# Kernel optimization log

Measured on AMD Instinct MI355X. Metric: run time of the kernel, lower is better.

The kernel has to match this reference:

```python
import jax, jax.numpy as jnp
import numpy as np

B, N, DIN, DOUT, H = 4, 2048, 256, 256, 4
HD = DOUT // H
NEG_SLOPE = 0.2


def setup_inputs() -> dict:
    key = jax.random.key(0)
    k1, k2, k3, k4, k5 = jax.random.split(key, 5)
    x = jax.random.normal(k1, (B, N, DIN), dtype=jnp.float32)
    adj = jax.random.randint(k2, (B, N, N), 0, 2).astype(jnp.float32)
    # ensure self-loops so every softmax row has at least one valid entry
    adj = jnp.maximum(adj, jnp.eye(N, dtype=jnp.float32)[None])
    # xavier-uniform-ish scales
    w_bound = float(np.sqrt(6.0 / (DIN + DOUT)))
    a_bound = float(np.sqrt(6.0 / (1 + HD)))
    W = jax.random.uniform(k3, (DOUT, DIN), jnp.float32, -w_bound, w_bound)
    a_src = jax.random.uniform(k4, (H, HD), jnp.float32, -a_bound, a_bound)
    a_dst = jax.random.uniform(k5, (H, HD), jnp.float32, -a_bound, a_bound)
    return {"x": x, "adj": adj, "W": W, "a_src": a_src, "a_dst": a_dst}


def reference(x, adj, W, a_src, a_dst):
    b, n, _ = x.shape
    h = (x @ W.T).reshape(b, n, H, HD)                      # [B,N,H,HD]
    s_src = jnp.einsum('bnhd,hd->bnh', h, a_src)            # [B,N,H]
    s_dst = jnp.einsum('bnhd,hd->bnh', h, a_dst)            # [B,N,H]
    # e[b,i,j,h] = leaky_relu(s_src[b,i,h] + s_dst[b,j,h])
    e = jax.nn.leaky_relu(s_src[:, :, None, :] + s_dst[:, None, :, :], NEG_SLOPE)
    e = jnp.where(adj[..., None] == 0, -jnp.inf, e)         # [B,N,N,H]
    alpha = jax.nn.softmax(e, axis=2)                       # softmax over j (dropout is identity at eval)
    out = jnp.einsum('bijh,bjhd->bihd', alpha, h)           # weighted aggregate
    return out.reshape(b, n, DOUT)
```

## Files before the change

kernel.cpp:

```cpp
#include <hip/hip_runtime.h>
#include <math.h>

#define Bb   4
#define Nn   2048
#define Dd   256
#define Hh   4
#define HDd  64
#define BN   (Bb * Nn)

typedef float v4f __attribute__((ext_vector_type(4)));
typedef short v8s __attribute__((ext_vector_type(8)));

__device__ __forceinline__ unsigned rne_bf16(float f) {
    unsigned u = __float_as_uint(f);
    u += 0x7fffu + ((u >> 16) & 1u);
    return u >> 16;
}

__global__ __launch_bounds__(256, 2) void k_gemm(const float* __restrict__ x,
                                                 const float* __restrict__ W,
                                                 const float* __restrict__ a_src,
                                                 const float* __restrict__ a_dst,
                                                 const float* __restrict__ adj,
                                                 unsigned short* __restrict__ hbf,
                                                 float* __restrict__ ssrc,
                                                 float* __restrict__ sdst,
                                                 unsigned long long* __restrict__ bitadj) {
    __shared__ __align__(16) unsigned short xs[2][64 * 72];
    __shared__ __align__(16) unsigned short wsm[2][64 * 72];
    __shared__ float asd[128];

    const int bid0 = (int)blockIdx.x;
    if (bid0 & 1) {
        const int gw = (bid0 >> 1) * 4 + ((int)threadIdx.x >> 6);
        const int lane = (int)threadIdx.x & 63;
#pragma unroll 1
        for (int w = gw * 4; w < 262144; w += 2048 * 4) {
            float v0 = adj[(size_t)((w + 0) >> 5) * 2048 + ((w + 0) & 31) * 64 + lane];
            float v1 = adj[(size_t)((w + 1) >> 5) * 2048 + ((w + 1) & 31) * 64 + lane];
            float v2 = adj[(size_t)((w + 2) >> 5) * 2048 + ((w + 2) & 31) * 64 + lane];
            float v3 = adj[(size_t)((w + 3) >> 5) * 2048 + ((w + 3) & 31) * 64 + lane];
            unsigned long long m0 = __ballot(v0 != 0.0f);
            unsigned long long m1 = __ballot(v1 != 0.0f);
            unsigned long long m2 = __ballot(v2 != 0.0f);
            unsigned long long m3 = __ballot(v3 != 0.0f);
            if (lane == 0) {
                bitadj[w + 0] = m0;
                bitadj[w + 1] = m1;
                bitadj[w + 2] = m2;
                bitadj[w + 3] = m3;
            }
        }
        return;
    }

    const int g = bid0 >> 1;
    const int head = (g >> 2) & 3;
    const int mtile = (g & 3) + 4 * (g >> 4);
    const int tid = threadIdx.x;
    const int m0 = mtile * 64;
    const int n0 = head * 64;
    const int b = m0 >> 11;
    const int i0loc = m0 & 2047;

    if (tid < 128) {
        int sel = tid >> 6, d = tid & 63;
        asd[tid] = sel ? a_dst[n0 + d] : a_src[n0 + d];
    }

    const int wv = tid >> 6, ln = tid & 63, l15 = ln & 15, l4 = ln >> 4;
    const int mh = wv >> 1, nh = wv & 1;
    const int srow = tid >> 2, kq = (tid & 3) * 16;

    v4f acc[2][2];
#pragma unroll
    for (int gg = 0; gg < 2; ++gg)
#pragma unroll
        for (int t = 0; t < 2; ++t) acc[gg][t] = (v4f){0.f, 0.f, 0.f, 0.f};

    for (int st = 0; st < 4; ++st) {
        const int k0 = st * 64;
        __syncthreads();
        {
            float xf[16], wf[16];
            const float* xp = x + (size_t)(m0 + srow) * Dd + k0 + kq;
            const float* wp = W + (size_t)(n0 + srow) * Dd + k0 + kq;
#pragma unroll
            for (int q = 0; q < 4; ++q) {
                *(float4*)&xf[q * 4] = *(const float4*)(xp + q * 4);
                *(float4*)&wf[q * 4] = *(const float4*)(wp + q * 4);
            }
            unsigned xh[8], xl[8], wh[8], wl[8];
#pragma unroll
            for (int j = 0; j < 8; ++j) {
                unsigned h0 = rne_bf16(xf[2 * j]), h1 = rne_bf16(xf[2 * j + 1]);
                float l0 = xf[2 * j] - __uint_as_float(h0 << 16);
                float l1 = xf[2 * j + 1] - __uint_as_float(h1 << 16);
                xh[j] = h0 | (h1 << 16);
                xl[j] = rne_bf16(l0) | (rne_bf16(l1) << 16);
                unsigned g0 = rne_bf16(wf[2 * j]), g1 = rne_bf16(wf[2 * j + 1]);
                float m0f = wf[2 * j] - __uint_as_float(g0 << 16);
                float m1f = wf[2 * j + 1] - __uint_as_float(g1 << 16);
                wh[j] = g0 | (g1 << 16);
                wl[j] = rne_bf16(m0f) | (rne_bf16(m1f) << 16);
            }
            *(uint4*)(xs[0] + srow * 72 + kq)     = make_uint4(xh[0], xh[1], xh[2], xh[3]);
            *(uint4*)(xs[0] + srow * 72 + kq + 8) = make_uint4(xh[4], xh[5], xh[6], xh[7]);
            *(uint4*)(xs[1] + srow * 72 + kq)     = make_uint4(xl[0], xl[1], xl[2], xl[3]);
            *(uint4*)(xs[1] + srow * 72 + kq + 8) = make_uint4(xl[4], xl[5], xl[6], xl[7]);
            *(uint4*)(wsm[0] + srow * 72 + kq)     = make_uint4(wh[0], wh[1], wh[2], wh[3]);
            *(uint4*)(wsm[0] + srow * 72 + kq + 8) = make_uint4(wh[4], wh[5], wh[6], wh[7]);
            *(uint4*)(wsm[1] + srow * 72 + kq)     = make_uint4(wl[0], wl[1], wl[2], wl[3]);
            *(uint4*)(wsm[1] + srow * 72 + kq + 8) = make_uint4(wl[4], wl[5], wl[6], wl[7]);
        }
        __syncthreads();
        {
            v8s ah[2][2], al[2][2], bh_[2][2], bl_[2][2];
#pragma unroll
            for (int gg = 0; gg < 2; ++gg)
#pragma unroll
                for (int kh = 0; kh < 2; ++kh) {
                    int ro = (mh * 32 + gg * 16 + l15) * 72 + kh * 32 + l4 * 8;
                    ah[gg][kh] = *(const v8s*)(xs[0] + ro);
                    al[gg][kh] = *(const v8s*)(xs[1] + ro);
                }
#pragma unroll
            for (int t = 0; t < 2; ++t)
#pragma unroll
                for (int kh = 0; kh < 2; ++kh) {
                    int ro = (nh * 32 + t * 16 + l15) * 72 + kh * 32 + l4 * 8;
                    bh_[t][kh] = *(const v8s*)(wsm[0] + ro);
                    bl_[t][kh] = *(const v8s*)(wsm[1] + ro);
                }
#pragma unroll
            for (int gg = 0; gg < 2; ++gg)
#pragma unroll
                for (int t = 0; t < 2; ++t)
#pragma unroll
                    for (int kh = 0; kh < 2; ++kh) {
                        acc[gg][t] = __builtin_amdgcn_mfma_f32_16x16x32_bf16(ah[gg][kh], bh_[t][kh], acc[gg][t], 0, 0, 0);
                        acc[gg][t] = __builtin_amdgcn_mfma_f32_16x16x32_bf16(al[gg][kh], bh_[t][kh], acc[gg][t], 0, 0, 0);
                        acc[gg][t] = __builtin_amdgcn_mfma_f32_16x16x32_bf16(ah[gg][kh], bl_[t][kh], acc[gg][t], 0, 0, 0);
                    }
        }
    }

    __syncthreads();
    float* T = (float*)&xs[0][0];
#pragma unroll
    for (int gg = 0; gg < 2; ++gg)
#pragma unroll
        for (int t = 0; t < 2; ++t)
#pragma unroll
            for (int r = 0; r < 4; ++r) {
                int d = nh * 32 + t * 16 + l15;
                int m = mh * 32 + gg * 16 + l4 * 4 + r;
                T[d * 67 + m] = acc[gg][t][r];
            }
    __syncthreads();
    if (tid < 128) {
        int m = tid & 63, sel = tid >> 6;
        float s = 0.f;
#pragma unroll
        for (int d = 0; d < 64; ++d) s += T[d * 67 + m] * asd[sel * 64 + d];
        (sel ? sdst : ssrc)[(size_t)head * BN + (size_t)b * Nn + i0loc + m] = s;
        int dloc = tid >> 1, jh2 = tid & 1;
        const float* row = T + dloc * 67 + jh2 * 32;
        unsigned pk[16];
#pragma unroll
        for (int jj = 0; jj < 16; ++jj)
            pk[jj] = rne_bf16(row[jj * 2]) | (rne_bf16(row[jj * 2 + 1]) << 16);
        const int jb = (i0loc >> 5) + jh2;
        const int dt = dloc >> 4, fl = dloc & 15;
        unsigned short* rb = hbf +
            ((size_t)((b * 64 + jb) * 4 + head) * 2048 + dt * 512 + fl * 8);
        *(uint4*)(rb + 0 * 128) = make_uint4(pk[0],  pk[1],  pk[2],  pk[3]);
        *(uint4*)(rb + 1 * 128) = make_uint4(pk[4],  pk[5],  pk[6],  pk[7]);
        *(uint4*)(rb + 2 * 128) = make_uint4(pk[8],  pk[9],  pk[10], pk[11]);
        *(uint4*)(rb + 3 * 128) = make_uint4(pk[12], pk[13], pk[14], pk[15]);
    }
}

__global__ __launch_bounds__(512, 4) void k_aggr(const unsigned short* __restrict__ hbf,
                                                 const unsigned long long* __restrict__ bitadj,
                                                 const float* __restrict__ ssrc,
                                                 const float* __restrict__ sdst,
                                                 float* __restrict__ out) {
    __shared__ __align__(16) unsigned short Btile[2][2][2048];
    __shared__ __align__(16) float dtab[2048 * 2];
    __shared__ __align__(16) float red[4][64][20];

    const int tid = threadIdx.x;
    const int bid = (int)blockIdx.x;
    const int xcd  = bid & 7;
    const int h    = xcd >> 1;
    const int bpar = xcd & 1;
    const int q    = bid >> 3;
    const int b    = ((q & 1) << 1) | bpar;
    const int itile = q >> 1;
    const int i0 = itile * 64;

    const int wv   = tid >> 6;
    const int isub = wv >> 1;
    const int jp   = wv & 1;
    const int ln = tid & 63, l15 = ln & 15, l4 = ln >> 4;

    const int spar = tid >> 8;
    const int soff = tid & 255;

    {
        const int j4 = tid * 4;
        float4 sv = *(const float4*)(sdst + (size_t)h * BN + (size_t)b * Nn + j4);
        float4 o0 = make_float4(__expf(sv.x), __expf(0.2f * sv.x),
                                __expf(sv.y), __expf(0.2f * sv.y));
        float4 o1 = make_float4(__expf(sv.z), __expf(0.2f * sv.z),
                                __expf(sv.w), __expf(0.2f * sv.w));
        *(float4*)&dtab[j4 * 2]     = o0;
        *(float4*)&dtab[j4 * 2 + 4] = o1;
    }

    const int irow = i0 + isub * 16 + l15;
    const float ss = ssrc[(size_t)h * BN + (size_t)b * Nn + irow];
    const float c1 = __expf(ss), c2 = __expf(0.2f * ss);
    const unsigned char* ajr = (const unsigned char*)bitadj +
        ((size_t)b * Nn + irow) * 256;
    const unsigned short* sbase = hbf +
        ((size_t)(b * 64 * 4) + h) * 2048 + (size_t)soff * 8;
    const float* dtb = dtab + l4 * 16;

    const v8s ones = {0x3F80, 0x3F80, 0x3F80, 0x3F80, 0x3F80, 0x3F80, 0x3F80, 0x3F80};

    v4f acc0 = (v4f){0.f, 0.f, 0.f, 0.f}, acc1 = acc0, acc2 = acc0, acc3 = acc0, zac = acc0;
    uint4 stg;
    unsigned mA, mB;

#define GENFRAG(dst, M_, dd_) do {                                            \
        const float4 q0_ = *(const float4*)((dd_) + 0);                       \
        const float4 q1_ = *(const float4*)((dd_) + 4);                       \
        const float4 q2_ = *(const float4*)((dd_) + 8);                       \
        const float4 q3_ = *(const float4*)((dd_) + 12);                      \
        float w0_ = ((M_) & 1u)   ? fmaxf(c1 * q0_.x, c2 * q0_.y) : 0.f;      \
        float w1_ = ((M_) & 2u)   ? fmaxf(c1 * q0_.z, c2 * q0_.w) : 0.f;      \
        float w2_ = ((M_) & 4u)   ? fmaxf(c1 * q1_.x, c2 * q1_.y) : 0.f;      \
        float w3_ = ((M_) & 8u)   ? fmaxf(c1 * q1_.z, c2 * q1_.w) : 0.f;      \
        float w4_ = ((M_) & 16u)  ? fmaxf(c1 * q2_.x, c2 * q2_.y) : 0.f;      \
        float w5_ = ((M_) & 32u)  ? fmaxf(c1 * q2_.z, c2 * q2_.w) : 0.f;      \
        float w6_ = ((M_) & 64u)  ? fmaxf(c1 * q3_.x, c2 * q3_.y) : 0.f;      \
        float w7_ = ((M_) & 128u) ? fmaxf(c1 * q3_.z, c2 * q3_.w) : 0.f;      \
        union { v8s v; unsigned u[4]; } P_;                                   \
        asm("v_cvt_pk_bf16_f32 %0, %1, %2" : "=v"(P_.u[0]) : "v"(w0_), "v"(w1_)); \
        asm("v_cvt_pk_bf16_f32 %0, %1, %2" : "=v"(P_.u[1]) : "v"(w2_), "v"(w3_)); \
        asm("v_cvt_pk_bf16_f32 %0, %1, %2" : "=v"(P_.u[2]) : "v"(w4_), "v"(w5_)); \
        asm("v_cvt_pk_bf16_f32 %0, %1, %2" : "=v"(P_.u[3]) : "v"(w6_), "v"(w7_)); \
        dst = P_.v;                                                           \
    } while (0)

#define COMPUTE(JC_, M_, btp) do {                                            \
        const unsigned short* bp_ = (btp);                                    \
        v8s bf0_ = *(const v8s*)(bp_ + 0 * 512 + ln * 8);                     \
        v8s bf1_ = *(const v8s*)(bp_ + 1 * 512 + ln * 8);                     \
        v8s bf2_ = *(const v8s*)(bp_ + 2 * 512 + ln * 8);                     \
        v8s bf3_ = *(const v8s*)(bp_ + 3 * 512 + ln * 8);                     \
        const float* dd_ = dtb + (JC_) * 64;                                  \
        v8s afr_;                                                             \
        GENFRAG(afr_, M_, dd_);                                               \
        acc0 = __builtin_amdgcn_mfma_f32_16x16x32_bf16(afr_, bf0_, acc0, 0, 0, 0); \
        acc1 = __builtin_amdgcn_mfma_f32_16x16x32_bf16(afr_, bf1_, acc1, 0, 0, 0); \
        acc2 = __builtin_amdgcn_mfma_f32_16x16x32_bf16(afr_, bf2_, acc2, 0, 0, 0); \
        acc3 = __builtin_amdgcn_mfma_f32_16x16x32_bf16(afr_, bf3_, acc3, 0, 0, 0); \
        zac  = __builtin_amdgcn_mfma_f32_16x16x32_bf16(afr_, ones, zac,  0, 0, 0); \
    } while (0)

    stg = *(const uint4*)(sbase + (size_t)spar * 8192);
    mA = ajr[jp * 4 + l4];
    *(uint4*)&Btile[0][spar][soff * 8] = stg;
    __syncthreads();

#pragma unroll 1
    for (int rr = 0; rr < 32; rr += 2) {
        {
            const int sjc = (2 * rr + 2 + spar) & 63;
            stg = *(const uint4*)(sbase + (size_t)sjc * 8192);
            mB = ajr[((2 * rr + 2 + jp) & 63) * 4 + l4];
            __builtin_amdgcn_sched_barrier(0);
            COMPUTE(2 * rr + jp, mA, Btile[0][jp]);
            *(uint4*)&Btile[1][spar][soff * 8] = stg;
            __syncthreads();
        }
        {
            const int sjc = (2 * rr + 4 + spar) & 63;
            stg = *(const uint4*)(sbase + (size_t)sjc * 8192);
            mA = ajr[((2 * rr + 4 + jp) & 63) * 4 + l4];
            __builtin_amdgcn_sched_barrier(0);
            COMPUTE(2 * rr + 2 + jp, mB, Btile[1][jp]);
            *(uint4*)&Btile[0][spar][soff * 8] = stg;
            __syncthreads();
        }
    }

#undef GENFRAG
#undef COMPUTE

    if (jp) {
        float* rp = &red[isub][ln][0];
        *(v4f*)(rp + 0)  = acc0;
        *(v4f*)(rp + 4)  = acc1;
        *(v4f*)(rp + 8)  = acc2;
        *(v4f*)(rp + 12) = acc3;
        *(v4f*)(rp + 16) = zac;
    }
    __syncthreads();
    if (!jp) {
        const float* rp = &red[isub][ln][0];
        acc0 += *(const v4f*)(rp + 0);
        acc1 += *(const v4f*)(rp + 4);
        acc2 += *(const v4f*)(rp + 8);
        acc3 += *(const v4f*)(rp + 12);
        zac  += *(const v4f*)(rp + 16);
        float* op = out + ((size_t)b * Nn + i0 + isub * 16 + l4 * 4) * Dd + h * HDd + l15;
#pragma unroll
        for (int r = 0; r < 4; ++r) {
            float zi = 1.f / zac[r];
            op[(size_t)r * Dd + 0]  = acc0[r] * zi;
            op[(size_t)r * Dd + 16] = acc1[r] * zi;
            op[(size_t)r * Dd + 32] = acc2[r] * zi;
            op[(size_t)r * Dd + 48] = acc3[r] * zi;
        }
    }
}

extern "C" void kernel_launch(void* const* d_in, const int* in_sizes, int n_in,
                              void* d_out, int out_size, void* d_ws, size_t ws_size,
                              hipStream_t stream) {
    const float* x     = (const float*)d_in[0];
    const float* adj   = (const float*)d_in[1];
    const float* W     = (const float*)d_in[2];
    const float* a_src = (const float*)d_in[3];
    const float* a_dst = (const float*)d_in[4];
    float* out = (float*)d_out;

    unsigned short* hbf = (unsigned short*)d_ws;
    float* ssrc = (float*)(hbf + (size_t)Bb * Nn * Dd);
    float* sdst = ssrc + (size_t)Hh * BN;
    unsigned long long* bitadj = (unsigned long long*)(sdst + (size_t)Hh * BN);

    k_gemm<<<dim3(1024), dim3(256), 0, stream>>>(x, W, a_src, a_dst, adj,
                                                 hbf, ssrc, sdst, bitadj);
    k_aggr<<<dim3(512), dim3(512), 0, stream>>>(hbf, bitadj, ssrc, sdst, out);
}
```

Before: 138.8 us.

## Stage four j-chunks per barrier in aggregation loop to halve syncs

The aggregation loop now loads four 32-column B chunks per stage (two uint4 per thread) into a doubled shared-memory tile, and each wave computes two chunks between barriers. This halves the number of __syncthreads and global-load rounds while keeping double buffering. In exchange it uses twice the Btile LDS (which could reduce occupancy) and more staging registers.

```diff
diff --git a/kernel.cpp b/kernel.cpp
--- a/kernel.cpp
+++ b/kernel.cpp
@@ -186,7 +186,7 @@
                                                  const float* __restrict__ ssrc,
                                                  const float* __restrict__ sdst,
                                                  float* __restrict__ out) {
-    __shared__ __align__(16) unsigned short Btile[2][2][2048];
+    __shared__ __align__(16) unsigned short Btile[2][4][2048];
     __shared__ __align__(16) float dtab[2048 * 2];
     __shared__ __align__(16) float red[4][64][20];
 
@@ -205,8 +205,8 @@
     const int jp   = wv & 1;
     const int ln = tid & 63, l15 = ln & 15, l4 = ln >> 4;
 
-    const int spar = tid >> 8;
-    const int soff = tid & 255;
+    const int ri   = (tid >> 7) & 3;
+    const int soff = (tid & 127) * 16;
 
     {
         const int j4 = tid * 4;
@@ -224,14 +224,14 @@
     const float c1 = __expf(ss), c2 = __expf(0.2f * ss);
     const unsigned char* ajr = (const unsigned char*)bitadj +
         ((size_t)b * Nn + irow) * 256;
-    const unsigned short* sbase = hbf +
-        ((size_t)(b * 64 * 4) + h) * 2048 + (size_t)soff * 8;
+    const unsigned short* sb2 = hbf +
+        ((size_t)(b * 64 * 4) + h) * 2048 + soff;
     const float* dtb = dtab + l4 * 16;
 
     const v8s ones = {0x3F80, 0x3F80, 0x3F80, 0x3F80, 0x3F80, 0x3F80, 0x3F80, 0x3F80};
 
     v4f acc0 = (v4f){0.f, 0.f, 0.f, 0.f}, acc1 = acc0, acc2 = acc0, acc3 = acc0, zac = acc0;
-    uint4 stg;
+    uint4 stg0, stg1;
     unsigned mA, mB;
 
 #define GENFRAG(dst, M_, dd_) do {                                            \
@@ -271,31 +271,29 @@
         zac  = __builtin_amdgcn_mfma_f32_16x16x32_bf16(afr_, ones, zac,  0, 0, 0); \
     } while (0)
 
-    stg = *(const uint4*)(sbase + (size_t)spar * 8192);
+    stg0 = *(const uint4*)(sb2 + (size_t)ri * 8192);
+    stg1 = *(const uint4*)(sb2 + (size_t)ri * 8192 + 8);
     mA = ajr[jp * 4 + l4];
-    *(uint4*)&Btile[0][spar][soff * 8] = stg;
+    mB = ajr[(2 + jp) * 4 + l4];
+    *(uint4*)&Btile[0][ri][soff]     = stg0;
+    *(uint4*)&Btile[0][ri][soff + 8] = stg1;
     __syncthreads();
 
 #pragma unroll 1
-    for (int rr = 0; rr < 32; rr += 2) {
-        {
-            const int sjc = (2 * rr + 2 + spar) & 63;
-            stg = *(const uint4*)(sbase + (size_t)sjc * 8192);
-            mB = ajr[((2 * rr + 2 + jp) & 63) * 4 + l4];
-            __builtin_amdgcn_sched_barrier(0);
-            COMPUTE(2 * rr + jp, mA, Btile[0][jp]);
-            *(uint4*)&Btile[1][spar][soff * 8] = stg;
-            __syncthreads();
-        }
-        {
-            const int sjc = (2 * rr + 4 + spar) & 63;
-            stg = *(const uint4*)(sbase + (size_t)sjc * 8192);
-            mA = ajr[((2 * rr + 4 + jp) & 63) * 4 + l4];
-            __builtin_amdgcn_sched_barrier(0);
-            COMPUTE(2 * rr + 2 + jp, mB, Btile[1][jp]);
-            *(uint4*)&Btile[0][spar][soff * 8] = stg;
-            __syncthreads();
-        }
+    for (int sr = 0; sr < 16; ++sr) {
+        const int buf = sr & 1;
+        const int jq = ((sr + 1) & 15) * 4;
+        stg0 = *(const uint4*)(sb2 + (size_t)(jq + ri) * 8192);
+        stg1 = *(const uint4*)(sb2 + (size_t)(jq + ri) * 8192 + 8);
+        const unsigned mA2 = ajr[(jq + jp) * 4 + l4];
+        const unsigned mB2 = ajr[(jq + 2 + jp) * 4 + l4];
+        __builtin_amdgcn_sched_barrier(0);
+        COMPUTE(4 * sr + jp,     mA, Btile[buf][jp]);
+        COMPUTE(4 * sr + 2 + jp, mB, Btile[buf][2 + jp]);
+        *(uint4*)&Btile[buf ^ 1][ri][soff]     = stg0;
+        *(uint4*)&Btile[buf ^ 1][ri][soff + 8] = stg1;
+        mA = mA2; mB = mB2;
+        __syncthreads();
     }
 
 #undef GENFRAG
```

Result: no change. 137.9 us (median of 2 runs) (-0.6%).
